# Kernel tuning notes

Hardware: AMD Instinct MI355X
Metric: run time of the kernel (lower is better)

## Reference

```python
import jax, jax.numpy as jnp
import numpy as np

B, S = 32, 1            # decode: one new token per sequence
H, KVH, D = 32, 8, 128  # GQA: 32 query heads, 8 kv heads
HID = 4096
MAX_SEQ = 2048
CUR_POS = MAX_SEQ - 1   # decode position (static, mirrors int(position_ids[0].item()))
GROUPS = H // KVH
EPS = 1e-6
LAYER_IDX = 0


def setup_inputs() -> dict:
    key = jax.random.key(0)
    ks = jax.random.split(key, 8)
    s = 0.02
    x = jax.random.normal(ks[0], (B, S, HID), jnp.float32)
    wq = jax.random.normal(ks[1], (H * D, HID), jnp.float32) * s
    wk = jax.random.normal(ks[2], (KVH * D, HID), jnp.float32) * s
    wv = jax.random.normal(ks[3], (KVH * D, HID), jnp.float32) * s
    wo = jax.random.normal(ks[4], (HID, H * D), jnp.float32) * s
    q_norm_w = jnp.ones((D,), jnp.float32)
    k_norm_w = jnp.ones((D,), jnp.float32)
    # standard HF-style RoPE tables: [MAX_SEQ, D]
    inv_freq = 1.0 / (10000.0 ** (jnp.arange(0, D, 2, dtype=jnp.float32) / D))
    pos = jnp.arange(MAX_SEQ, dtype=jnp.float32)
    freqs = pos[:, None] * inv_freq[None, :]          # [MAX_SEQ, D/2]
    emb = jnp.concatenate([freqs, freqs], axis=-1)    # [MAX_SEQ, D]
    cos, sin = jnp.cos(emb), jnp.sin(emb)
    k_cache = jax.random.normal(ks[5], (1, B, MAX_SEQ, KVH, D), jnp.float32) * 0.1
    v_cache = jax.random.normal(ks[6], (1, B, MAX_SEQ, KVH, D), jnp.float32) * 0.1
    position_ids = jnp.full((B, S), CUR_POS, dtype=jnp.int32)
    return dict(x=x, wq=wq, wk=wk, wv=wv, wo=wo, q_norm_w=q_norm_w,
                k_norm_w=k_norm_w, cos=cos, sin=sin,
                k_cache=k_cache, v_cache=v_cache, position_ids=position_ids)


def _rms_norm(x, w):
    return w * (x * jax.lax.rsqrt(jnp.mean(x * x, axis=-1, keepdims=True) + EPS))


def _apply_rope(x, cos, sin, position_ids):
    # x: [B, heads, S, D]; cos/sin: [MAX_SEQ, D]; position_ids: [B, S]
    c = cos[position_ids][:, None]  # [B,1,S,D]
    s = sin[position_ids][:, None]
    x1, x2 = x[..., : D // 2], x[..., D // 2:]
    rotated = jnp.concatenate([-x2, x1], axis=-1)
    return x * c + rotated * s


def reference(x, wq, wk, wv, wo, q_norm_w, k_norm_w, cos, sin,
              k_cache, v_cache, position_ids):
    # projections (Linear with weight [out,in], no bias)
    q = (x @ wq.T).reshape(B, S, H, D).transpose(0, 2, 1, 3)      # [B,H,S,D]
    k = (x @ wk.T).reshape(B, S, KVH, D).transpose(0, 2, 1, 3)    # [B,KVH,S,D]
    v = (x @ wv.T).reshape(B, S, KVH, D).transpose(0, 2, 1, 3)
    # per-head QK RMSNorm + RoPE
    q = _apply_rope(_rms_norm(q, q_norm_w), cos, sin, position_ids)
    k = _apply_rope(_rms_norm(k, k_norm_w), cos, sin, position_ids)
    # decode branch: write new K/V at CUR_POS, read cache[:CUR_POS+1]
    k_cache = k_cache.at[LAYER_IDX, :, CUR_POS].set(k[:, :, 0, :].transpose(0, 1, 2))
    v_cache = v_cache.at[LAYER_IDX, :, CUR_POS].set(v[:, :, 0, :])
    keys = k_cache[LAYER_IDX, :, : CUR_POS + 1].transpose(0, 2, 1, 3)    # [B,KVH,T,D]
    values = v_cache[LAYER_IDX, :, : CUR_POS + 1].transpose(0, 2, 1, 3)  # [B,KVH,T,D]
    # GQA expand (repeat_interleave on head dim)
    keys = jnp.repeat(keys, GROUPS, axis=1)      # [B,H,T,D]
    values = jnp.repeat(values, GROUPS, axis=1)  # [B,H,T,D]
    # SDPA (non-causal for decode: query is last position)
    scale = 1.0 / jnp.sqrt(jnp.float32(D))
    scores = jnp.einsum('bhqd,bhkd->bhqk', q, keys) * scale
    attn = jax.nn.softmax(scores, axis=-1)
    out = jnp.einsum('bhqk,bhkd->bhqd', attn, values)   # [B,H,S,D]
    out = out.transpose(0, 2, 1, 3).reshape(B, S, H * D)
    return out @ wo.T
```

## Files before the change

### kernel.cpp

```cpp
#include <hip/hip_runtime.h>
#include <math.h>

#define B_    32
#define H_    32
#define KVH_  8
#define D_    128
#define HID_  4096
#define SEQ_  2048
#define CUR_  2047
#define QKVF_ 6144
#define SCALE_ 0.08838834764831845f

__global__ __launch_bounds__(256) void transpose_x(const float* __restrict__ x,
                                                   float* __restrict__ xT4) {
    int i = blockIdx.x * 256 + threadIdx.x;
    int i4 = i & 3;
    int b  = (i >> 2) & 31;
    int kb = i >> 7;
    xT4[i] = x[b * HID_ + kb * 4 + i4];
}

__global__ __launch_bounds__(256) void gemm_qkv(const float* __restrict__ wq,
                                                const float* __restrict__ wk,
                                                const float* __restrict__ wv,
                                                const float* __restrict__ xT4,
                                                float* __restrict__ qkv) {
    int b = threadIdx.x & 31;
    int f = blockIdx.x * 8 + (threadIdx.x >> 5);
    const float* wrow;
    if (f < 4096)       wrow = wq + (size_t)f * HID_;
    else if (f < 5120)  wrow = wk + (size_t)(f - 4096) * HID_;
    else                wrow = wv + (size_t)(f - 5120) * HID_;
    const float4* w4p = (const float4*)wrow;
    const float4* x4p = (const float4*)xT4;
    float ax = 0.f, ay = 0.f, az = 0.f, aw = 0.f;
#pragma unroll 8
    for (int kb = 0; kb < 1024; ++kb) {
        float4 w  = w4p[kb];
        float4 xv = x4p[kb * 32 + b];
        ax = fmaf(w.x, xv.x, ax);
        ay = fmaf(w.y, xv.y, ay);
        az = fmaf(w.z, xv.z, az);
        aw = fmaf(w.w, xv.w, aw);
    }
    qkv[b * QKVF_ + f] = (ax + ay) + (az + aw);
}

__global__ __launch_bounds__(256) void norm_rope(const float* __restrict__ qkv,
                                                 const float* __restrict__ qnw,
                                                 const float* __restrict__ knw,
                                                 const float* __restrict__ cosT,
                                                 const float* __restrict__ sinT,
                                                 const int* __restrict__ pos_ids,
                                                 float* __restrict__ qhat,
                                                 float* __restrict__ khat) {
    int u = blockIdx.x * 4 + (threadIdx.x >> 6);
    int l = threadIdx.x & 63;
    int b  = u / 40;
    int hh = u % 40;
    bool isq = hh < 32;
    const float* src = qkv + b * QKVF_ + (isq ? hh * D_ : HID_ + (hh - 32) * D_);
    float v0 = src[l];
    float v1 = src[l + 64];
    float ss = v0 * v0 + v1 * v1;
#pragma unroll
    for (int m = 1; m <= 32; m <<= 1) ss += __shfl_xor(ss, m, 64);
    float r = rsqrtf(ss * (1.0f / 128.0f) + 1e-6f);
    const float* nw = isq ? qnw : knw;
    float n0 = v0 * r * nw[l];
    float n1 = v1 * r * nw[l + 64];
    int pos = pos_ids[b];
    const float* cp = cosT + (size_t)pos * D_;
    const float* sp = sinT + (size_t)pos * D_;
    float o0 = n0 * cp[l]      - n1 * sp[l];
    float o1 = n1 * cp[l + 64] + n0 * sp[l + 64];
    if (isq) { o0 *= SCALE_; o1 *= SCALE_; }
    float* dst = isq ? (qhat + (size_t)(b * 32 + hh) * D_)
                     : (khat + (size_t)(b * 8 + (hh - 32)) * D_);
    dst[l]      = o0;
    dst[l + 64] = o1;
}

__global__ __launch_bounds__(1024) void attn(const float* __restrict__ qhat,
                                             const float* __restrict__ khat,
                                             const float* __restrict__ qkv,
                                             const float* __restrict__ kcache,
                                             const float* __restrict__ vcache,
                                             float* __restrict__ aoutT4) {
    __shared__ float sl[4 * SEQ_];
    __shared__ float mscr[4][4], lscr[4][4];
    int b    = blockIdx.x >> 3;
    int kvh  = blockIdx.x & 7;
    int wave = threadIdx.x >> 6;
    int lane = threadIdx.x & 63;
    int g    = lane >> 5;
    int dl   = lane & 31;
    int d0   = dl * 4;

    float4 q4[4];
#pragma unroll
    for (int h = 0; h < 4; ++h)
        q4[h] = *(const float4*)(qhat + (size_t)((b * 32 + kvh * 4 + h) * D_) + d0);

    const float* kbase = kcache + ((size_t)b * SEQ_ * KVH_ + kvh) * D_;
    const float* knew  = khat + (size_t)(b * 8 + kvh) * D_;
    int t0 = wave * 128 + g;

#pragma unroll 4
    for (int it = 0; it < 64; ++it) {
        int row = t0 + it * 2;
        const float* kr = (row == CUR_) ? knew : (kbase + (size_t)row * (KVH_ * D_));
        float4 k4 = *(const float4*)(kr + d0);
#pragma unroll
        for (int h = 0; h < 4; ++h) {
            float p = fmaf(q4[h].x, k4.x,
                      fmaf(q4[h].y, k4.y,
                      fmaf(q4[h].z, k4.z, q4[h].w * k4.w)));
            p += __shfl_xor(p, 1, 64);
            p += __shfl_xor(p, 2, 64);
            p += __shfl_xor(p, 4, 64);
            p += __shfl_xor(p, 8, 64);
            p += __shfl_xor(p, 16, 64);
            if (dl == 0) sl[h * SEQ_ + row] = p;
        }
    }
    __syncthreads();

    {
        int hg = threadIdx.x >> 8;
        int t  = threadIdx.x & 255;
        float m = -3.402823466e38f;
#pragma unroll
        for (int j = 0; j < 8; ++j) m = fmaxf(m, sl[hg * SEQ_ + t + j * 256]);
#pragma unroll
        for (int msk = 1; msk <= 32; msk <<= 1) m = fmaxf(m, __shfl_xor(m, msk, 64));
        int wg = (threadIdx.x >> 6) & 3;
        if (lane == 0) mscr[hg][wg] = m;
        __syncthreads();
        m = fmaxf(fmaxf(mscr[hg][0], mscr[hg][1]), fmaxf(mscr[hg][2], mscr[hg][3]));
        float lsum = 0.f;
#pragma unroll
        for (int j = 0; j < 8; ++j) {
            int idx = hg * SEQ_ + t + j * 256;
            float e = __expf(sl[idx] - m);
            sl[idx] = e;
            lsum += e;
        }
#pragma unroll
        for (int msk = 1; msk <= 32; msk <<= 1) lsum += __shfl_xor(lsum, msk, 64);
        if (lane == 0) lscr[hg][wg] = lsum;
        __syncthreads();
    }

    const float* vbase = vcache + ((size_t)b * SEQ_ * KVH_ + kvh) * D_;
    const float* vnew  = qkv + b * QKVF_ + 5120 + kvh * D_;
    float4 acc[4];
#pragma unroll
    for (int h = 0; h < 4; ++h) acc[h] = make_float4(0.f, 0.f, 0.f, 0.f);
#pragma unroll 4
    for (int it = 0; it < 64; ++it) {
        int row = t0 + it * 2;
        const float* vr = (row == CUR_) ? vnew : (vbase + (size_t)row * (KVH_ * D_));
        float4 v4 = *(const float4*)(vr + d0);
#pragma unroll
        for (int h = 0; h < 4; ++h) {
            float pv = sl[h * SEQ_ + row];
            acc[h].x = fmaf(pv, v4.x, acc[h].x);
            acc[h].y = fmaf(pv, v4.y, acc[h].y);
            acc[h].z = fmaf(pv, v4.z, acc[h].z);
            acc[h].w = fmaf(pv, v4.w, acc[h].w);
        }
    }
#pragma unroll
    for (int h = 0; h < 4; ++h) {
        acc[h].x += __shfl_xor(acc[h].x, 32, 64);
        acc[h].y += __shfl_xor(acc[h].y, 32, 64);
        acc[h].z += __shfl_xor(acc[h].z, 32, 64);
        acc[h].w += __shfl_xor(acc[h].w, 32, 64);
    }
    __syncthreads();
    if (g == 0) {
#pragma unroll
        for (int h = 0; h < 4; ++h)
            *(float4*)(sl + wave * 512 + h * 128 + d0) = acc[h];
    }
    __syncthreads();
    if (threadIdx.x < 512) {
        int h = threadIdx.x >> 7;
        int d = threadIdx.x & 127;
        float o = 0.f;
#pragma unroll
        for (int w = 0; w < 16; ++w) o += sl[w * 512 + h * 128 + d];
        o /= (lscr[h][0] + lscr[h][1] + lscr[h][2] + lscr[h][3]);
        int f = (kvh * 4 + h) * D_ + d;
        aoutT4[(size_t)(f >> 2) * 128 + b * 4 + (f & 3)] = o;
    }
}

__global__ __launch_bounds__(256) void gemm_o(const float* __restrict__ wo,
                                              const float* __restrict__ aT4,
                                              float* __restrict__ out) {
    int b = threadIdx.x & 31;
    int f = blockIdx.x * 8 + (threadIdx.x >> 5);
    const float4* w4p = (const float4*)(wo + (size_t)f * HID_);
    const float4* x4p = (const float4*)aT4;
    float ax = 0.f, ay = 0.f, az = 0.f, aw = 0.f;
#pragma unroll 8
    for (int kb = 0; kb < 1024; ++kb) {
        float4 w  = w4p[kb];
        float4 xv = x4p[kb * 32 + b];
        ax = fmaf(w.x, xv.x, ax);
        ay = fmaf(w.y, xv.y, ay);
        az = fmaf(w.z, xv.z, az);
        aw = fmaf(w.w, xv.w, aw);
    }
    out[b * HID_ + f] = (ax + ay) + (az + aw);
}

extern "C" void kernel_launch(void* const* d_in, const int* in_sizes, int n_in,
                              void* d_out, int out_size, void* d_ws, size_t ws_size,
                              hipStream_t stream) {
    const float* x      = (const float*)d_in[0];
    const float* wq     = (const float*)d_in[1];
    const float* wk     = (const float*)d_in[2];
    const float* wv     = (const float*)d_in[3];
    const float* wo     = (const float*)d_in[4];
    const float* qnw    = (const float*)d_in[5];
    const float* knw    = (const float*)d_in[6];
    const float* cosT   = (const float*)d_in[7];
    const float* sinT   = (const float*)d_in[8];
    const float* kcache = (const float*)d_in[9];
    const float* vcache = (const float*)d_in[10];
    const int*   pos    = (const int*)d_in[11];
    float* out = (float*)d_out;
    float* ws  = (float*)d_ws;

    float* xT4  = ws;
    float* qkv  = ws + 131072;
    float* qhat = ws + 327680;
    float* khat = ws + 458752;
    float* aT4  = ws + 491520;

    transpose_x<<<512, 256, 0, stream>>>(x, xT4);
    gemm_qkv<<<768, 256, 0, stream>>>(wq, wk, wv, xT4, qkv);
    norm_rope<<<320, 256, 0, stream>>>(qkv, qnw, knw, cosT, sinT, pos, qhat, khat);
    attn<<<256, 1024, 0, stream>>>(qhat, khat, qkv, kcache, vcache, aT4);
    gemm_o<<<512, 256, 0, stream>>>(wo, aT4, out);
}
```

Baseline: 982.0 us.

## Split-KV flash-decode attention with LDS DMA, combine pass, and untransposed GEMMs

Replaces the single-pass attention kernel (one 1024-thread block per batch/kv-head) with a split-KV flash-decoding kernel. It uses 8 sequence chunks per head and streams K/V tiles into swizzled LDS via global_load_lds with an online softmax. A separate combine kernel merges the partial results. The transpose_x kernel is removed and both GEMMs now read activations row-major with a new thread mapping. This raises parallelism for the attention step, which reads 128 MB of KV cache, at the cost of an extra launch and partial-result traffic.

```diff
diff --git a/kernel.cpp b/kernel.cpp
--- a/kernel.cpp
+++ b/kernel.cpp
@@ -1,5 +1,6 @@
 #include <hip/hip_runtime.h>
 #include <math.h>
+#include <stdint.h>
 
 #define B_    32
 #define H_    32
@@ -7,43 +8,45 @@
 #define D_    128
 #define HID_  4096
 #define SEQ_  2048
-#define CUR_  2047
 #define QKVF_ 6144
 #define SCALE_ 0.08838834764831845f
-
-__global__ __launch_bounds__(256) void transpose_x(const float* __restrict__ x,
-                                                   float* __restrict__ xT4) {
-    int i = blockIdx.x * 256 + threadIdx.x;
-    int i4 = i & 3;
-    int b  = (i >> 2) & 31;
-    int kb = i >> 7;
-    xT4[i] = x[b * HID_ + kb * 4 + i4];
+#define NCHUNK 8
+#define CHUNK_ 256
+#define TROWS  32
+#define NTILE  8
+
+typedef const __attribute__((address_space(1))) uint32_t* gp_t;
+typedef __attribute__((address_space(3))) uint32_t* lp_t;
+
+__device__ __forceinline__ void dma16(const float* src, float* ldsdst) {
+    __builtin_amdgcn_global_load_lds((gp_t)src, (lp_t)ldsdst, 16, 0, 0);
 }
 
 __global__ __launch_bounds__(256) void gemm_qkv(const float* __restrict__ wq,
                                                 const float* __restrict__ wk,
                                                 const float* __restrict__ wv,
-                                                const float* __restrict__ xT4,
+                                                const float* __restrict__ x,
                                                 float* __restrict__ qkv) {
-    int b = threadIdx.x & 31;
-    int f = blockIdx.x * 8 + (threadIdx.x >> 5);
+    int w = threadIdx.x >> 6, lane = threadIdx.x & 63;
+    int f = blockIdx.x * 8 + (lane & 7);
+    int bb = w * 8 + (lane >> 3);
     const float* wrow;
-    if (f < 4096)       wrow = wq + (size_t)f * HID_;
-    else if (f < 5120)  wrow = wk + (size_t)(f - 4096) * HID_;
-    else                wrow = wv + (size_t)(f - 5120) * HID_;
-    const float4* w4p = (const float4*)wrow;
-    const float4* x4p = (const float4*)xT4;
+    if (f < HID_)             wrow = wq + (size_t)f * HID_;
+    else if (f < HID_ + 1024) wrow = wk + (size_t)(f - HID_) * HID_;
+    else                      wrow = wv + (size_t)(f - HID_ - 1024) * HID_;
+    const float4* wp = (const float4*)wrow;
+    const float4* xp = (const float4*)(x + (size_t)bb * HID_);
     float ax = 0.f, ay = 0.f, az = 0.f, aw = 0.f;
 #pragma unroll 8
-    for (int kb = 0; kb < 1024; ++kb) {
-        float4 w  = w4p[kb];
-        float4 xv = x4p[kb * 32 + b];
-        ax = fmaf(w.x, xv.x, ax);
-        ay = fmaf(w.y, xv.y, ay);
-        az = fmaf(w.z, xv.z, az);
-        aw = fmaf(w.w, xv.w, aw);
-    }
-    qkv[b * QKVF_ + f] = (ax + ay) + (az + aw);
+    for (int k = 0; k < 1024; ++k) {
+        float4 wv4 = wp[k];
+        float4 xv4 = xp[k];
+        ax = fmaf(wv4.x, xv4.x, ax);
+        ay = fmaf(wv4.y, xv4.y, ay);
+        az = fmaf(wv4.z, xv4.z, az);
+        aw = fmaf(wv4.w, xv4.w, aw);
+    }
+    qkv[bb * QKVF_ + f] = (ax + ay) + (az + aw);
 }
 
 __global__ __launch_bounds__(256) void norm_rope(const float* __restrict__ qkv,
@@ -81,140 +84,196 @@
     dst[l + 64] = o1;
 }
 
-__global__ __launch_bounds__(1024) void attn(const float* __restrict__ qhat,
-                                             const float* __restrict__ khat,
-                                             const float* __restrict__ qkv,
-                                             const float* __restrict__ kcache,
-                                             const float* __restrict__ vcache,
-                                             float* __restrict__ aoutT4) {
-    __shared__ float sl[4 * SEQ_];
-    __shared__ float mscr[4][4], lscr[4][4];
-    int b    = blockIdx.x >> 3;
-    int kvh  = blockIdx.x & 7;
-    int wave = threadIdx.x >> 6;
-    int lane = threadIdx.x & 63;
-    int g    = lane >> 5;
-    int dl   = lane & 31;
-    int d0   = dl * 4;
-
-    float4 q4[4];
-#pragma unroll
-    for (int h = 0; h < 4; ++h)
-        q4[h] = *(const float4*)(qhat + (size_t)((b * 32 + kvh * 4 + h) * D_) + d0);
+__global__ __launch_bounds__(256) void attn_fd(const float* __restrict__ qhat,
+                                               const float* __restrict__ khat,
+                                               const float* __restrict__ qkv,
+                                               const float* __restrict__ kcache,
+                                               const float* __restrict__ vcache,
+                                               float* __restrict__ part) {
+    __shared__ float Kl[TROWS * 128];
+    __shared__ float Vl[TROWS * 128];
+    __shared__ float Ql[4 * 128];
+    __shared__ float Pb[4 * TROWS];
+    __shared__ float Ms[16];
+    __shared__ float Ls[16];
+
+    int tid = threadIdx.x;
+    int w = tid >> 6, lane = tid & 63;
+    int bi = blockIdx.x;
+    int chunk = bi & 7, kvh = (bi >> 3) & 7, b = bi >> 6;
 
     const float* kbase = kcache + ((size_t)b * SEQ_ * KVH_ + kvh) * D_;
-    const float* knew  = khat + (size_t)(b * 8 + kvh) * D_;
-    int t0 = wave * 128 + g;
-
-#pragma unroll 4
-    for (int it = 0; it < 64; ++it) {
-        int row = t0 + it * 2;
-        const float* kr = (row == CUR_) ? knew : (kbase + (size_t)row * (KVH_ * D_));
-        float4 k4 = *(const float4*)(kr + d0);
-#pragma unroll
-        for (int h = 0; h < 4; ++h) {
-            float p = fmaf(q4[h].x, k4.x,
-                      fmaf(q4[h].y, k4.y,
-                      fmaf(q4[h].z, k4.z, q4[h].w * k4.w)));
-            p += __shfl_xor(p, 1, 64);
-            p += __shfl_xor(p, 2, 64);
-            p += __shfl_xor(p, 4, 64);
-            p += __shfl_xor(p, 8, 64);
-            p += __shfl_xor(p, 16, 64);
-            if (dl == 0) sl[h * SEQ_ + row] = p;
-        }
-    }
-    __syncthreads();
-
-    {
-        int hg = threadIdx.x >> 8;
-        int t  = threadIdx.x & 255;
-        float m = -3.402823466e38f;
-#pragma unroll
-        for (int j = 0; j < 8; ++j) m = fmaxf(m, sl[hg * SEQ_ + t + j * 256]);
-#pragma unroll
-        for (int msk = 1; msk <= 32; msk <<= 1) m = fmaxf(m, __shfl_xor(m, msk, 64));
-        int wg = (threadIdx.x >> 6) & 3;
-        if (lane == 0) mscr[hg][wg] = m;
+    const float* vbase = vcache + ((size_t)b * SEQ_ * KVH_ + kvh) * D_;
+    const float* knew  = khat + (size_t)(b * KVH_ + kvh) * D_;
+    const float* vnew  = qkv + b * QKVF_ + HID_ + KVH_ * D_ + kvh * D_;
+    int row0 = chunk * CHUNK_;
+
+    if (tid < 128) {
+        int h = tid >> 5, tl = tid & 31;
+        float4 qv = ((const float4*)(qhat + (size_t)((b * H_ + kvh * 4 + h) * D_)))[tl];
+        int phys = (tl & 28) | ((tl + (tl >> 2)) & 3);
+        *(float4*)(Ql + h * 128 + phys * 4) = qv;
+    }
+
+#pragma unroll
+    for (int p = 0; p < 4; ++p) {
+        int i = tid + p * 256;
+        int r = i >> 5, c = i & 31;
+        int l = (c & 24) | ((c ^ r) & 7);
+        int grow = row0 + r;
+        const float* src = (grow == SEQ_ - 1) ? (knew + l * 4)
+                          : (kbase + (size_t)grow * (KVH_ * D_) + l * 4);
+        dma16(src, Kl + i * 4);
+    }
+
+    float m_run = -3.4e38f, lsum = 0.f, O0 = 0.f, O1 = 0.f;
+    int r8 = lane >> 3, d8 = lane & 7;
+    int srow = w * 8 + r8;
+    int kswz = srow & 7;
+
+    for (int tile = 0; tile < NTILE; ++tile) {
+#pragma unroll
+        for (int p = 0; p < 4; ++p) {
+            int i = tid + p * 256;
+            int r = i >> 5, c = i & 31;
+            int grow = row0 + tile * TROWS + r;
+            const float* src = (grow == SEQ_ - 1) ? (vnew + c * 4)
+                              : (vbase + (size_t)grow * (KVH_ * D_) + c * 4);
+            dma16(src, Vl + i * 4);
+        }
+        asm volatile("s_waitcnt vmcnt(4) lgkmcnt(0)" ::: "memory");
+        __builtin_amdgcn_s_barrier();
+
+        float s0 = 0.f, s1 = 0.f, s2 = 0.f, s3 = 0.f;
+#pragma unroll
+        for (int t = 0; t < 4; ++t) {
+            int l = d8 * 4 + t;
+            int phys = (l & 24) | ((l ^ kswz) & 7);
+            float4 k4 = *(const float4*)(Kl + srow * 128 + phys * 4);
+            int qp = d8 * 4 + ((t + d8) & 3);
+            float4 qa = *(const float4*)(Ql + 0 * 128 + qp * 4);
+            float4 qb = *(const float4*)(Ql + 1 * 128 + qp * 4);
+            float4 qc = *(const float4*)(Ql + 2 * 128 + qp * 4);
+            float4 qd = *(const float4*)(Ql + 3 * 128 + qp * 4);
+            s0 = fmaf(qa.x, k4.x, fmaf(qa.y, k4.y, fmaf(qa.z, k4.z, fmaf(qa.w, k4.w, s0))));
+            s1 = fmaf(qb.x, k4.x, fmaf(qb.y, k4.y, fmaf(qb.z, k4.z, fmaf(qb.w, k4.w, s1))));
+            s2 = fmaf(qc.x, k4.x, fmaf(qc.y, k4.y, fmaf(qc.z, k4.z, fmaf(qc.w, k4.w, s2))));
+            s3 = fmaf(qd.x, k4.x, fmaf(qd.y, k4.y, fmaf(qd.z, k4.z, fmaf(qd.w, k4.w, s3))));
+        }
+#pragma unroll
+        for (int m = 1; m <= 4; m <<= 1) {
+            s0 += __shfl_xor(s0, m, 64);
+            s1 += __shfl_xor(s1, m, 64);
+            s2 += __shfl_xor(s2, m, 64);
+            s3 += __shfl_xor(s3, m, 64);
+        }
+        int hsel = d8 & 3;
+        float s = (hsel == 0) ? s0 : (hsel == 1) ? s1 : (hsel == 2) ? s2 : s3;
+        float mx = s;
+        mx = fmaxf(mx, __shfl_xor(mx, 8, 64));
+        mx = fmaxf(mx, __shfl_xor(mx, 16, 64));
+        mx = fmaxf(mx, __shfl_xor(mx, 32, 64));
+        float pt = __expf(s - mx);
+        if (d8 < 4) Pb[hsel * TROWS + srow] = pt;
+        float ps = pt;
+        ps += __shfl_xor(ps, 8, 64);
+        ps += __shfl_xor(ps, 16, 64);
+        ps += __shfl_xor(ps, 32, 64);
+        if (r8 == 0 && d8 < 4) { Ms[w * 4 + d8] = mx; Ls[w * 4 + d8] = ps; }
+
         __syncthreads();
-        m = fmaxf(fmaxf(mscr[hg][0], mscr[hg][1]), fmaxf(mscr[hg][2], mscr[hg][3]));
-        float lsum = 0.f;
-#pragma unroll
-        for (int j = 0; j < 8; ++j) {
-            int idx = hg * SEQ_ + t + j * 256;
-            float e = __expf(sl[idx] - m);
-            sl[idx] = e;
-            lsum += e;
-        }
-#pragma unroll
-        for (int msk = 1; msk <= 32; msk <<= 1) lsum += __shfl_xor(lsum, msk, 64);
-        if (lane == 0) lscr[hg][wg] = lsum;
+
+        if (tile + 1 < NTILE) {
+#pragma unroll
+            for (int p = 0; p < 4; ++p) {
+                int i = tid + p * 256;
+                int r = i >> 5, c = i & 31;
+                int l = (c & 24) | ((c ^ r) & 7);
+                int grow = row0 + (tile + 1) * TROWS + r;
+                const float* src = (grow == SEQ_ - 1) ? (knew + l * 4)
+                                  : (kbase + (size_t)grow * (KVH_ * D_) + l * 4);
+                dma16(src, Kl + i * 4);
+            }
+        }
+
+        float mw0 = Ms[0 * 4 + w], mw1 = Ms[1 * 4 + w], mw2 = Ms[2 * 4 + w], mw3 = Ms[3 * 4 + w];
+        float mt = fmaxf(fmaxf(mw0, mw1), fmaxf(mw2, mw3));
+        float m_new = fmaxf(m_run, mt);
+        float alpha = __expf(m_run - m_new);
+        O0 *= alpha; lsum *= alpha; O1 *= alpha;
+        m_run = m_new;
+        float bw0 = __expf(mw0 - m_new), bw1 = __expf(mw1 - m_new);
+        float bw2 = __expf(mw2 - m_new), bw3 = __expf(mw3 - m_new);
+        lsum = fmaf(Ls[0 * 4 + w], bw0, lsum);
+        lsum = fmaf(Ls[1 * 4 + w], bw1, lsum);
+        lsum = fmaf(Ls[2 * 4 + w], bw2, lsum);
+        lsum = fmaf(Ls[3 * 4 + w], bw3, lsum);
+#pragma unroll
+        for (int g2 = 0; g2 < 8; ++g2) {
+            float bw = (g2 < 2) ? bw0 : (g2 < 4) ? bw1 : (g2 < 6) ? bw2 : bw3;
+            float4 s4 = *(const float4*)(Pb + w * TROWS + g2 * 4);
+#pragma unroll
+            for (int j = 0; j < 4; ++j) {
+                float pv = ((j == 0) ? s4.x : (j == 1) ? s4.y : (j == 2) ? s4.z : s4.w) * bw;
+                float2 v2 = *(const float2*)(Vl + (g2 * 4 + j) * 128 + lane * 2);
+                O0 = fmaf(pv, v2.x, O0);
+                O1 = fmaf(pv, v2.y, O1);
+            }
+        }
         __syncthreads();
     }
 
-    const float* vbase = vcache + ((size_t)b * SEQ_ * KVH_ + kvh) * D_;
-    const float* vnew  = qkv + b * QKVF_ + 5120 + kvh * D_;
-    float4 acc[4];
-#pragma unroll
-    for (int h = 0; h < 4; ++h) acc[h] = make_float4(0.f, 0.f, 0.f, 0.f);
-#pragma unroll 4
-    for (int it = 0; it < 64; ++it) {
-        int row = t0 + it * 2;
-        const float* vr = (row == CUR_) ? vnew : (vbase + (size_t)row * (KVH_ * D_));
-        float4 v4 = *(const float4*)(vr + d0);
-#pragma unroll
-        for (int h = 0; h < 4; ++h) {
-            float pv = sl[h * SEQ_ + row];
-            acc[h].x = fmaf(pv, v4.x, acc[h].x);
-            acc[h].y = fmaf(pv, v4.y, acc[h].y);
-            acc[h].z = fmaf(pv, v4.z, acc[h].z);
-            acc[h].w = fmaf(pv, v4.w, acc[h].w);
-        }
-    }
-#pragma unroll
-    for (int h = 0; h < 4; ++h) {
-        acc[h].x += __shfl_xor(acc[h].x, 32, 64);
-        acc[h].y += __shfl_xor(acc[h].y, 32, 64);
-        acc[h].z += __shfl_xor(acc[h].z, 32, 64);
-        acc[h].w += __shfl_xor(acc[h].w, 32, 64);
-    }
-    __syncthreads();
-    if (g == 0) {
-#pragma unroll
-        for (int h = 0; h < 4; ++h)
-            *(float4*)(sl + wave * 512 + h * 128 + d0) = acc[h];
-    }
-    __syncthreads();
-    if (threadIdx.x < 512) {
-        int h = threadIdx.x >> 7;
-        int d = threadIdx.x & 127;
-        float o = 0.f;
-#pragma unroll
-        for (int w = 0; w < 16; ++w) o += sl[w * 512 + h * 128 + d];
-        o /= (lscr[h][0] + lscr[h][1] + lscr[h][2] + lscr[h][3]);
-        int f = (kvh * 4 + h) * D_ + d;
-        aoutT4[(size_t)(f >> 2) * 128 + b * 4 + (f & 3)] = o;
-    }
+    size_t base = ((size_t)((b * KVH_ + kvh) * 4 + w) * NCHUNK + chunk) * 130;
+    *(float2*)(part + base + 2 * lane) = make_float2(O0, O1);
+    if (lane == 0) { part[base + 128] = m_run; part[base + 129] = lsum; }
+}
+
+__global__ __launch_bounds__(64) void combine(const float* __restrict__ part,
+                                              float* __restrict__ aout) {
+    int bi = blockIdx.x;
+    int b = bi >> 5, hg = bi & 31;
+    int kvh = hg >> 2, hl = hg & 3;
+    int lane = threadIdx.x;
+    size_t base0 = (size_t)((b * KVH_ + kvh) * 4 + hl) * NCHUNK * 130;
+    float mstar = -3.4e38f;
+#pragma unroll
+    for (int c = 0; c < NCHUNK; ++c) mstar = fmaxf(mstar, part[base0 + c * 130 + 128]);
+    float L = 0.f, A0 = 0.f, A1 = 0.f;
+#pragma unroll
+    for (int c = 0; c < NCHUNK; ++c) {
+        float mc = part[base0 + c * 130 + 128];
+        float lc = part[base0 + c * 130 + 129];
+        float e = __expf(mc - mstar);
+        L = fmaf(lc, e, L);
+        float2 oc = *(const float2*)(part + base0 + c * 130 + 2 * lane);
+        A0 = fmaf(oc.x, e, A0);
+        A1 = fmaf(oc.y, e, A1);
+    }
+    float inv = 1.0f / L;
+    size_t o = (size_t)b * HID_ + hg * D_ + 2 * lane;
+    aout[o]     = A0 * inv;
+    aout[o + 1] = A1 * inv;
 }
 
 __global__ __launch_bounds__(256) void gemm_o(const float* __restrict__ wo,
-                                              const float* __restrict__ aT4,
+                                              const float* __restrict__ aout,
                                               float* __restrict__ out) {
-    int b = threadIdx.x & 31;
-    int f = blockIdx.x * 8 + (threadIdx.x >> 5);
-    const float4* w4p = (const float4*)(wo + (size_t)f * HID_);
-    const float4* x4p = (const float4*)aT4;
+    int w = threadIdx.x >> 6, lane = threadIdx.x & 63;
+    int f = blockIdx.x * 8 + (lane & 7);
+    int bb = w * 8 + (lane >> 3);
+    const float4* wp = (const float4*)(wo + (size_t)f * HID_);
+    const float4* xp = (const float4*)(aout + (size_t)bb * HID_);
     float ax = 0.f, ay = 0.f, az = 0.f, aw = 0.f;
 #pragma unroll 8
-    for (int kb = 0; kb < 1024; ++kb) {
-        float4 w  = w4p[kb];
-        float4 xv = x4p[kb * 32 + b];
-        ax = fmaf(w.x, xv.x, ax);
-        ay = fmaf(w.y, xv.y, ay);
-        az = fmaf(w.z, xv.z, az);
-        aw = fmaf(w.w, xv.w, aw);
-    }
-    out[b * HID_ + f] = (ax + ay) + (az + aw);
+    for (int k = 0; k < 1024; ++k) {
+        float4 wv4 = wp[k];
+        float4 xv4 = xp[k];
+        ax = fmaf(wv4.x, xv4.x, ax);
+        ay = fmaf(wv4.y, xv4.y, ay);
+        az = fmaf(wv4.z, xv4.z, az);
+        aw = fmaf(wv4.w, xv4.w, aw);
+    }
+    out[bb * HID_ + f] = (ax + ay) + (az + aw);
 }
 
 extern "C" void kernel_launch(void* const* d_in, const int* in_sizes, int n_in,
@@ -235,15 +294,15 @@
     float* out = (float*)d_out;
     float* ws  = (float*)d_ws;
 
-    float* xT4  = ws;
-    float* qkv  = ws + 131072;
-    float* qhat = ws + 327680;
-    float* khat = ws + 458752;
-    float* aT4  = ws + 491520;
-
-    transpose_x<<<512, 256, 0, stream>>>(x, xT4);
-    gemm_qkv<<<768, 256, 0, stream>>>(wq, wk, wv, xT4, qkv);
+    float* qkv  = ws;
+    float* qhat = ws + 196608;
+    float* khat = ws + 327680;
+    float* part = ws + 360448;
+    float* aout = ws + 1425408;
+
+    gemm_qkv<<<768, 256, 0, stream>>>(wq, wk, wv, x, qkv);
     norm_rope<<<320, 256, 0, stream>>>(qkv, qnw, knw, cosT, sinT, pos, qhat, khat);
-    attn<<<256, 1024, 0, stream>>>(qhat, khat, qkv, kcache, vcache, aT4);
-    gemm_o<<<512, 256, 0, stream>>>(wo, aT4, out);
-}
+    attn_fd<<<2048, 256, 0, stream>>>(qhat, khat, qkv, kcache, vcache, part);
+    combine<<<1024, 64, 0, stream>>>(part, aout);
+    gemm_o<<<512, 256, 0, stream>>>(wo, aout, out);
+}
```

After: 1.275 ms. +29.8%, slower.
